# Kernel optimization log

Hardware: AMD Instinct MI355X
Metric: run time of the kernel (lower is better)

Reference implementation:

```python
import jax, jax.numpy as jnp
import numpy as np

VOCAB, EMBED, FILT, LABELS = 30522, 256, 256, 50
B, S = 32, 4096

def setup_inputs() -> dict:
    key = jax.random.key(0)
    k0, k1, k2, k3, k4 = jax.random.split(key, 5)
    return {
        "input_ids": jax.random.randint(k0, (B, S), 0, VOCAB),
        "emb_table": jax.random.normal(k1, (VOCAB, EMBED), dtype=jnp.float32) * 0.02,
        "conv_w": jax.random.normal(k2, (FILT, EMBED, 4), dtype=jnp.float32) * 0.05,  # (out_ch, in_ch, k)
        "conv_b": jnp.zeros((FILT,), dtype=jnp.float32),
        "U_w": jax.random.normal(k3, (LABELS, FILT), dtype=jnp.float32) * 0.05,  # torch Linear weight layout
        "final_w": jax.random.normal(k4, (LABELS, FILT), dtype=jnp.float32) * 0.05,
        "final_b": jnp.zeros((LABELS,), dtype=jnp.float32),
    }

def reference(input_ids, emb_table, conv_w, conv_b, U_w, final_w, final_b):
    # Embedding lookup: (B, S, E) -> NCH layout (B, E, S)
    x = jnp.take(emb_table, input_ids, axis=0).transpose(0, 2, 1)
    # Conv1d(kernel=4, padding=2): output length S+1
    h = jax.lax.conv_general_dilated(
        x, conv_w, window_strides=(1,), padding=[(2, 2)],
        dimension_numbers=("NCH", "OIH", "NCH"))
    H = jnp.tanh(h + conv_b[None, :, None]).transpose(0, 2, 1)  # (B, S+1, F)
    # Per-label attention: softmax over the sequence dimension
    scores = jnp.einsum("bsf,lf->bsl", H, U_w)          # (B, S+1, L)
    alpha = jax.nn.softmax(scores, axis=1)
    m = jnp.einsum("bsl,bsf->blf", alpha, H)             # (B, L, F)
    logits = jnp.sum(m * final_w[None], axis=2) + final_b  # (B, L)
    return logits
```

## Files before the change

### kernel.cpp

```cpp
#include <hip/hip_runtime.h>
#include <hip/hip_bf16.h>
#include <stdint.h>

#define BDIM 32
#define SDIM 4096
#define SP1  4097
#define EDIM 256
#define FDIM 256
#define LDIM 50
#define TTILE 128
#define NT    32

typedef __attribute__((ext_vector_type(8))) short bf16x8v;
typedef __attribute__((ext_vector_type(4))) float f32x4;

__device__ __forceinline__ unsigned short f2bf(float f) {
    union { float f; uint32_t u; } v; v.f = f;
    uint32_t u = v.u;
    uint32_t r = (u + 0x7fffu + ((u >> 16) & 1u)) >> 16;
    return (unsigned short)r;
}

__device__ __forceinline__ float tanh_fast(float x) {
    float e = __expf(2.0f * x);
    float r = __builtin_amdgcn_rcpf(e + 1.0f);
    return fmaf(-2.0f, r, 1.0f);
}

__device__ __forceinline__ uint32_t pack_bf2(float lo, float hi) {
    union { __hip_bfloat162 v; uint32_t u; } cv;
    cv.v = __halves2bfloat162(__float2bfloat16(lo), __float2bfloat16(hi));
    return cv.u;
}

__device__ __forceinline__ void load_lds16(const void* g, uint32_t* l) {
    __builtin_amdgcn_global_load_lds(
        (const __attribute__((address_space(1))) uint32_t*)g,
        (__attribute__((address_space(3))) uint32_t*)l, 16, 0, 0);
}

__global__ void prep_all(const float* __restrict__ emb, const float* __restrict__ conv_w,
                         const float* __restrict__ U_w, const float* __restrict__ final_w,
                         unsigned short* __restrict__ embb, unsigned short* __restrict__ Wb2,
                         unsigned short* __restrict__ W2k, float* __restrict__ Wt01,
                         uint32_t* __restrict__ zp)
{
    int o = blockIdx.x * 256 + threadIdx.x;
    size_t eo = (size_t)o * 8;
    if (eo < (size_t)30522 * 256) {
        float4 v0 = *(const float4*)(emb + eo);
        float4 v1 = *(const float4*)(emb + eo + 4);
        union { unsigned short u[8]; uint4 q; } pk;
        pk.u[0] = f2bf(v0.x); pk.u[1] = f2bf(v0.y); pk.u[2] = f2bf(v0.z); pk.u[3] = f2bf(v0.w);
        pk.u[4] = f2bf(v1.x); pk.u[5] = f2bf(v1.y); pk.u[6] = f2bf(v1.z); pk.u[7] = f2bf(v1.w);
        *(uint4*)(embb + eo) = pk.q;
    }
    if (o < 262144) {
        int kk = o & 1023, f = o >> 10;
        int e = kk & 255, k = kk >> 8;
        int g = kk >> 5, h4 = (kk >> 3) & 3, j = kk & 7;
        Wb2[((size_t)(g * 4 + h4) * 256 + f) * 8 + j] = f2bf(conv_w[f * 1024 + e * 4 + k]);
    }
    if (o < 32768) {
        int j = o & 7, c = (o >> 3) & 127, g = o >> 10;
        int k = g * 8 + j, l = c & 63;
        float v = 0.f;
        if (l < LDIM) v = (c < 64) ? U_w[l * FDIM + k] : final_w[l * FDIM + k];
        W2k[o] = f2bf(v);
    }
    if (o < 65536) {
        int f = o & 255, e = o >> 8;
        Wt01[(size_t)o * 2]     = conv_w[f * 1024 + e * 4];
        Wt01[(size_t)o * 2 + 1] = conv_w[f * 1024 + e * 4 + 1];
    }
    if (o < 128) zp[o] = 0;
}

__global__ __launch_bounds__(256, 2) void fused_kernel(
    const int* __restrict__ ids, const unsigned short* __restrict__ embb,
    const unsigned short* __restrict__ Wb2, const float* __restrict__ conv_b,
    const unsigned short* __restrict__ W2k, const uint32_t* __restrict__ zp,
    float* __restrict__ part)
{
    __shared__ uint32_t xs[132 * 128];

    const int tid  = threadIdx.x;
    const int lane = tid & 63;
    const int wid  = tid >> 6;
    const int b    = blockIdx.y;
    const int tile = blockIdx.x;
    const int t0   = tile * TTILE;
    const int l15  = lane & 15;
    const int hi4  = lane >> 4;
    const int q    = lane & 31;
    const int half = lane >> 5;

    {
        int nid[17];
        #pragma unroll
        for (int j = 0; j < 17; ++j) {
            int r0 = wid * 2 + j * 8;
            int r  = r0 + half;
            int p  = t0 - 2 + r;
            nid[j] = -1;
            if (r0 < 131 && r < 131 && (unsigned)p < SDIM)
                nid[j] = ids[b * SDIM + p];
        }
        const unsigned short* zs = (const unsigned short*)zp + q * 8;
        #pragma unroll
        for (int j = 0; j < 17; ++j) {
            int r0 = wid * 2 + j * 8;
            if (r0 >= 131) continue;
            int r = r0 + half;
            const unsigned short* s = (nid[j] >= 0)
                ? embb + (size_t)nid[j] * EDIM + (((uint32_t)(q * 16) ^ ((uint32_t)(r & 7) << 4)) >> 1)
                : zs;
            load_lds16(s, &xs[r0 * 128]);
        }
    }
    __syncthreads();

    const int fbase = wid * 64;
    const unsigned short* afbase = Wb2 + (size_t)(hi4 * 256 + fbase + l15) * 8;

    f32x4 acc[4][8];
    #pragma unroll
    for (int a = 0; a < 4; ++a)
        #pragma unroll
        for (int n = 0; n < 8; ++n) acc[a][n] = (f32x4){0.f, 0.f, 0.f, 0.f};

    bf16x8v afc[4];
    #pragma unroll
    for (int a = 0; a < 4; ++a) afc[a] = *(const bf16x8v*)(afbase + a * 128);

    #pragma unroll 1
    for (int k = 0; k < 4; ++k) {
        uint32_t bb[8];
        #pragma unroll
        for (int n = 0; n < 8; ++n) {
            int r = n * 16 + l15 + k;
            bb[n] = (uint32_t)(r * 512) ^ (uint32_t)(hi4 * 16) ^ (uint32_t)((r & 7) << 4);
        }
        const unsigned short* afg = afbase + (size_t)k * 65536;
        #pragma unroll
        for (int es = 0; es < 8; ++es) {
            const unsigned short* nxt = (es < 7)
                ? (afg + (size_t)(es + 1) * 8192)
                : (afbase + (size_t)((k + 1) & 3) * 65536);
            bf16x8v afn[4];
            #pragma unroll
            for (int a = 0; a < 4; ++a) afn[a] = *(const bf16x8v*)(nxt + a * 128);

            bf16x8v bfr[8];
            #pragma unroll
            for (int n = 0; n < 8; ++n)
                bfr[n] = *(const bf16x8v*)((const char*)xs + (bb[n] ^ (uint32_t)(es * 64)));

            __builtin_amdgcn_s_setprio(1);
            #pragma unroll
            for (int a = 0; a < 4; ++a)
                #pragma unroll
                for (int n = 0; n < 8; ++n)
                    acc[a][n] = __builtin_amdgcn_mfma_f32_16x16x32_bf16(afc[a], bfr[n], acc[a][n], 0, 0, 0);
            __builtin_amdgcn_s_setprio(0);

            #pragma unroll
            for (int a = 0; a < 4; ++a) afc[a] = afn[a];
        }
    }
    __syncthreads();

    float4 cb[4];
    #pragma unroll
    for (int a = 0; a < 4; ++a)
        cb[a] = *(const float4*)(conv_b + fbase + a * 16 + hi4 * 4);
    #pragma unroll
    for (int n = 0; n < 8; ++n) {
        int tl = n * 16 + l15;
        uint32_t hb = (uint32_t)(tl * 512) ^ (uint32_t)(hi4 * 8)
                    ^ (uint32_t)(fbase * 2) ^ (uint32_t)((tl & 7) << 4);
        #pragma unroll
        for (int a = 0; a < 4; ++a) {
            f32x4 d = acc[a][n];
            uint2 pk;
            pk.x = pack_bf2(tanh_fast(d[0] + cb[a].x), tanh_fast(d[1] + cb[a].y));
            pk.y = pack_bf2(tanh_fast(d[2] + cb[a].z), tanh_fast(d[3] + cb[a].w));
            *(uint2*)((char*)xs + (hb ^ (uint32_t)(a * 32))) = pk;
        }
    }
    __syncthreads();

    const int cbase = wid * 16;
    f32x4 p2[8][2];
    #pragma unroll
    for (int m = 0; m < 8; ++m) { p2[m][0] = (f32x4){0,0,0,0}; p2[m][1] = (f32x4){0,0,0,0}; }

    uint32_t pb[8];
    #pragma unroll
    for (int m = 0; m < 8; ++m) {
        int sl = m * 16 + l15;
        pb[m] = (uint32_t)(sl * 512) ^ (uint32_t)(hi4 * 16) ^ (uint32_t)((sl & 7) << 4);
    }
    const unsigned short* wp0 = W2k + (size_t)(hi4 * 128 + cbase + l15) * 8;

    #pragma unroll
    for (int step = 0; step < 8; ++step) {
        bf16x8v ha[8], w2[2];
        #pragma unroll
        for (int m = 0; m < 8; ++m)
            ha[m] = *(const bf16x8v*)((const char*)xs + (pb[m] ^ (uint32_t)(step * 64)));
        w2[0] = *(const bf16x8v*)(wp0 + step * 4096);
        w2[1] = *(const bf16x8v*)(wp0 + 512 + step * 4096);
        __builtin_amdgcn_s_setprio(1);
        #pragma unroll
        for (int m = 0; m < 8; ++m) {
            p2[m][0] = __builtin_amdgcn_mfma_f32_16x16x32_bf16(ha[m], w2[0], p2[m][0], 0, 0, 0);
            p2[m][1] = __builtin_amdgcn_mfma_f32_16x16x32_bf16(ha[m], w2[1], p2[m][1], 0, 0, 0);
        }
        __builtin_amdgcn_s_setprio(0);
    }

    float mx = -1e30f;
    #pragma unroll
    for (int m = 0; m < 8; ++m)
        #pragma unroll
        for (int i = 0; i < 4; ++i)
            mx = fmaxf(mx, p2[m][0][i]);
    float se = 0.f, st = 0.f;
    #pragma unroll
    for (int m = 0; m < 8; ++m)
        #pragma unroll
        for (int i = 0; i < 4; ++i) {
            float e = __expf(p2[m][0][i] - mx);
            se += e;
            st += e * p2[m][1][i];
        }
    #pragma unroll
    for (int d = 16; d <= 32; d <<= 1) {
        float mo  = __shfl_xor(mx, d);
        float seo = __shfl_xor(se, d);
        float sto = __shfl_xor(st, d);
        float M  = fmaxf(mx, mo);
        float w0 = __expf(mx - M), w1 = __expf(mo - M);
        se = se * w0 + seo * w1;
        st = st * w0 + sto * w1;
        mx = M;
    }
    if (lane < 16) {
        int l = cbase + l15;
        if (l < LDIM) {
            size_t o = (((size_t)b * NT + tile) * LDIM + l) * 3;
            part[o] = mx; part[o + 1] = se; part[o + 2] = st;
        }
    }
}

__global__ __launch_bounds__(256) void final_kernel(
    const int* __restrict__ ids, const float* __restrict__ emb,
    const float* __restrict__ Wt01, const float* __restrict__ conv_b,
    const float* __restrict__ U_w, const float* __restrict__ final_w,
    const float* __restrict__ part, const float* __restrict__ final_b,
    float* __restrict__ out)
{
    __shared__ float x0[EDIM], x1[EDIM], hsh[FDIM], rsc[256], rtv[256];
    const int b = blockIdx.x, t = threadIdx.x;

    {
        int id0 = ids[b * SDIM + 4094];
        int id1 = ids[b * SDIM + 4095];
        x0[t] = emb[(size_t)id0 * EDIM + t];
        x1[t] = emb[(size_t)id1 * EDIM + t];
    }
    __syncthreads();

    {
        const float2* wt = (const float2*)Wt01;
        float a0 = 0.f, a1 = 0.f, a2 = 0.f, a3 = 0.f;
        #pragma unroll 4
        for (int e = 0; e < 256; e += 4) {
            float2 w0 = wt[(e + 0) * 256 + t];
            float2 w1 = wt[(e + 1) * 256 + t];
            float2 w2 = wt[(e + 2) * 256 + t];
            float2 w3 = wt[(e + 3) * 256 + t];
            a0 = fmaf(w0.x, x0[e + 0], fmaf(w0.y, x1[e + 0], a0));
            a1 = fmaf(w1.x, x0[e + 1], fmaf(w1.y, x1[e + 1], a1));
            a2 = fmaf(w2.x, x0[e + 2], fmaf(w2.y, x1[e + 2], a2));
            a3 = fmaf(w3.x, x0[e + 3], fmaf(w3.y, x1[e + 3], a3));
        }
        hsh[t] = tanhf(conv_b[t] + ((a0 + a1) + (a2 + a3)));
    }
    __syncthreads();

    {
        const int l = t & 63, c = t >> 6;
        float sc = 0.f, tv = 0.f;
        if (l < LDIM) {
            const float4* uw = (const float4*)(U_w + (size_t)l * FDIM + c * 64);
            const float4* fw = (const float4*)(final_w + (size_t)l * FDIM + c * 64);
            const float4* hh = (const float4*)(hsh + c * 64);
            #pragma unroll
            for (int i = 0; i < 16; ++i) {
                float4 h = hh[i], u = uw[i], w = fw[i];
                sc = fmaf(h.x, u.x, fmaf(h.y, u.y, fmaf(h.z, u.z, fmaf(h.w, u.w, sc))));
                tv = fmaf(h.x, w.x, fmaf(h.y, w.y, fmaf(h.z, w.z, fmaf(h.w, w.w, tv))));
            }
        }
        rsc[t] = sc; rtv[t] = tv;
    }
    __syncthreads();

    if (t < LDIM) {
        float sc = rsc[t] + rsc[t + 64] + rsc[t + 128] + rsc[t + 192];
        float tv = rtv[t] + rtv[t + 64] + rtv[t + 128] + rtv[t + 192];
        float mx = sc, se = 1.0f, st = tv;
        for (int c = 0; c < NT; ++c) {
            size_t o = (((size_t)b * NT + c) * LDIM + t) * 3;
            float mo = part[o], seo = part[o + 1], sto = part[o + 2];
            float M  = fmaxf(mx, mo);
            float w0 = __expf(mx - M), w1 = __expf(mo - M);
            se = se * w0 + seo * w1;
            st = st * w0 + sto * w1;
            mx = M;
        }
        out[b * LDIM + t] = st / se + final_b[t];
    }
}

extern "C" void kernel_launch(void* const* d_in, const int* in_sizes, int n_in,
                              void* d_out, int out_size, void* d_ws, size_t ws_size,
                              hipStream_t stream)
{
    const int*   ids     = (const int*)d_in[0];
    const float* emb     = (const float*)d_in[1];
    const float* conv_w  = (const float*)d_in[2];
    const float* conv_b  = (const float*)d_in[3];
    const float* U_w     = (const float*)d_in[4];
    const float* final_w = (const float*)d_in[5];
    const float* final_b = (const float*)d_in[6];

    char* ws = (char*)d_ws;
    size_t offE  = 0;
    size_t szE   = (size_t)30522 * 256 * 2;
    size_t offWb = offE + szE;
    size_t szWb  = 256 * 1024 * 2;
    size_t offW2 = offWb + szWb;
    size_t szW2  = 32768 * 2;
    size_t offWt = offW2 + szW2;
    size_t szWt  = 65536 * 2 * 4;
    size_t offZ  = offWt + szWt;
    size_t szZ   = 512;
    size_t offP  = offZ + szZ;

    unsigned short* embb = (unsigned short*)(ws + offE);
    unsigned short* Wb2  = (unsigned short*)(ws + offWb);
    unsigned short* W2k  = (unsigned short*)(ws + offW2);
    float*          Wt01 = (float*)(ws + offWt);
    uint32_t*       zp   = (uint32_t*)(ws + offZ);
    float*          prt  = (float*)(ws + offP);

    prep_all<<<3816, 256, 0, stream>>>(emb, conv_w, U_w, final_w, embb, Wb2, W2k, Wt01, zp);
    fused_kernel<<<dim3(NT, BDIM), 256, 0, stream>>>(ids, embb, Wb2, conv_b, W2k, zp, prt);
    final_kernel<<<BDIM, 256, 0, stream>>>(ids, emb, Wt01, conv_b, U_w, final_w,
                                           prt, final_b, (float*)d_out);
}
```

Baseline: 97.57 us.

## Fold final reduction into fused kernel via last-block atomic counter

Removes the separate final_kernel launch. Each batch gets one extra block that computes the tail-position conv and attention contribution. The last block to arrive, tracked by an atomic counter per batch, merges all partial softmax states and writes the output. This saves one kernel launch and the serialization between kernels, at the cost of threadfences, atomics and an extra block per batch row in the main grid.

After: 166.4 us. +70.6%, slower.

```diff
diff --git a/kernel.cpp b/kernel.cpp
--- a/kernel.cpp
+++ b/kernel.cpp
@@ -39,11 +39,18 @@
         (__attribute__((address_space(3))) uint32_t*)l, 16, 0, 0);
 }
 
+__device__ __forceinline__ void pstore(float* p, float v) {
+    __hip_atomic_store(p, v, __ATOMIC_RELAXED, __HIP_MEMORY_SCOPE_AGENT);
+}
+__device__ __forceinline__ float pload(const float* p) {
+    return __hip_atomic_load(p, __ATOMIC_RELAXED, __HIP_MEMORY_SCOPE_AGENT);
+}
+
 __global__ void prep_all(const float* __restrict__ emb, const float* __restrict__ conv_w,
                          const float* __restrict__ U_w, const float* __restrict__ final_w,
                          unsigned short* __restrict__ embb, unsigned short* __restrict__ Wb2,
                          unsigned short* __restrict__ W2k, float* __restrict__ Wt01,
-                         uint32_t* __restrict__ zp)
+                         uint32_t* __restrict__ zp, int* __restrict__ cnt)
 {
     int o = blockIdx.x * 256 + threadIdx.x;
     size_t eo = (size_t)o * 8;
@@ -74,255 +81,274 @@
         Wt01[(size_t)o * 2 + 1] = conv_w[f * 1024 + e * 4 + 1];
     }
     if (o < 128) zp[o] = 0;
+    if (o < BDIM) cnt[o] = 0;
 }
 
 __global__ __launch_bounds__(256, 2) void fused_kernel(
     const int* __restrict__ ids, const unsigned short* __restrict__ embb,
     const unsigned short* __restrict__ Wb2, const float* __restrict__ conv_b,
     const unsigned short* __restrict__ W2k, const uint32_t* __restrict__ zp,
-    float* __restrict__ part)
+    const float* __restrict__ Wt01, const float* __restrict__ emb,
+    const float* __restrict__ U_w, const float* __restrict__ final_w,
+    const float* __restrict__ final_b, float* __restrict__ part,
+    int* __restrict__ cnt, float* __restrict__ out)
 {
     __shared__ uint32_t xs[132 * 128];
+    __shared__ int lord;
 
     const int tid  = threadIdx.x;
     const int lane = tid & 63;
     const int wid  = tid >> 6;
     const int b    = blockIdx.y;
     const int tile = blockIdx.x;
-    const int t0   = tile * TTILE;
-    const int l15  = lane & 15;
-    const int hi4  = lane >> 4;
-    const int q    = lane & 31;
-    const int half = lane >> 5;
-
-    {
-        int nid[17];
-        #pragma unroll
-        for (int j = 0; j < 17; ++j) {
-            int r0 = wid * 2 + j * 8;
-            int r  = r0 + half;
-            int p  = t0 - 2 + r;
-            nid[j] = -1;
-            if (r0 < 131 && r < 131 && (unsigned)p < SDIM)
-                nid[j] = ids[b * SDIM + p];
-        }
-        const unsigned short* zs = (const unsigned short*)zp + q * 8;
-        #pragma unroll
-        for (int j = 0; j < 17; ++j) {
-            int r0 = wid * 2 + j * 8;
-            if (r0 >= 131) continue;
-            int r = r0 + half;
-            const unsigned short* s = (nid[j] >= 0)
-                ? embb + (size_t)nid[j] * EDIM + (((uint32_t)(q * 16) ^ ((uint32_t)(r & 7) << 4)) >> 1)
-                : zs;
-            load_lds16(s, &xs[r0 * 128]);
-        }
-    }
-    __syncthreads();
-
-    const int fbase = wid * 64;
-    const unsigned short* afbase = Wb2 + (size_t)(hi4 * 256 + fbase + l15) * 8;
-
-    f32x4 acc[4][8];
-    #pragma unroll
-    for (int a = 0; a < 4; ++a)
-        #pragma unroll
-        for (int n = 0; n < 8; ++n) acc[a][n] = (f32x4){0.f, 0.f, 0.f, 0.f};
-
-    bf16x8v afc[4];
-    #pragma unroll
-    for (int a = 0; a < 4; ++a) afc[a] = *(const bf16x8v*)(afbase + a * 128);
-
-    #pragma unroll 1
-    for (int k = 0; k < 4; ++k) {
-        uint32_t bb[8];
+
+    if (tile < NT) {
+        const int t0   = tile * TTILE;
+        const int l15  = lane & 15;
+        const int hi4  = lane >> 4;
+        const int q    = lane & 31;
+        const int half = lane >> 5;
+
+        {
+            int nid[17];
+            #pragma unroll
+            for (int j = 0; j < 17; ++j) {
+                int r0 = wid * 2 + j * 8;
+                int r  = r0 + half;
+                int p  = t0 - 2 + r;
+                nid[j] = -1;
+                if (r0 < 131 && r < 131 && (unsigned)p < SDIM)
+                    nid[j] = ids[b * SDIM + p];
+            }
+            const unsigned short* zs = (const unsigned short*)zp + q * 8;
+            #pragma unroll
+            for (int j = 0; j < 17; ++j) {
+                int r0 = wid * 2 + j * 8;
+                if (r0 >= 131) continue;
+                int r = r0 + half;
+                const unsigned short* s = (nid[j] >= 0)
+                    ? embb + (size_t)nid[j] * EDIM + (((uint32_t)(q * 16) ^ ((uint32_t)(r & 7) << 4)) >> 1)
+                    : zs;
+                load_lds16(s, &xs[r0 * 128]);
+            }
+        }
+        __syncthreads();
+
+        const int fbase = wid * 64;
+        const unsigned short* afbase = Wb2 + (size_t)(hi4 * 256 + fbase + l15) * 8;
+
+        f32x4 acc[4][8];
+        #pragma unroll
+        for (int a = 0; a < 4; ++a)
+            #pragma unroll
+            for (int n = 0; n < 8; ++n) acc[a][n] = (f32x4){0.f, 0.f, 0.f, 0.f};
+
+        bf16x8v afc[4];
+        #pragma unroll
+        for (int a = 0; a < 4; ++a) afc[a] = *(const bf16x8v*)(afbase + a * 128);
+
+        #pragma unroll 1
+        for (int k = 0; k < 4; ++k) {
+            uint32_t bb[8];
+            #pragma unroll
+            for (int n = 0; n < 8; ++n) {
+                int r = n * 16 + l15 + k;
+                bb[n] = (uint32_t)(r * 512) ^ (uint32_t)(hi4 * 16) ^ (uint32_t)((r & 7) << 4);
+            }
+            const unsigned short* afg = afbase + (size_t)k * 65536;
+            #pragma unroll
+            for (int es = 0; es < 8; ++es) {
+                const unsigned short* nxt = (es < 7)
+                    ? (afg + (size_t)(es + 1) * 8192)
+                    : (afbase + (size_t)((k + 1) & 3) * 65536);
+                bf16x8v afn[4];
+                #pragma unroll
+                for (int a = 0; a < 4; ++a) afn[a] = *(const bf16x8v*)(nxt + a * 128);
+
+                bf16x8v bfr[8];
+                #pragma unroll
+                for (int n = 0; n < 8; ++n)
+                    bfr[n] = *(const bf16x8v*)((const char*)xs + (bb[n] ^ (uint32_t)(es * 64)));
+
+                __builtin_amdgcn_s_setprio(1);
+                #pragma unroll
+                for (int a = 0; a < 4; ++a)
+                    #pragma unroll
+                    for (int n = 0; n < 8; ++n)
+                        acc[a][n] = __builtin_amdgcn_mfma_f32_16x16x32_bf16(afc[a], bfr[n], acc[a][n], 0, 0, 0);
+                __builtin_amdgcn_s_setprio(0);
+
+                #pragma unroll
+                for (int a = 0; a < 4; ++a) afc[a] = afn[a];
+            }
+        }
+        __syncthreads();
+
+        float4 cb[4];
+        #pragma unroll
+        for (int a = 0; a < 4; ++a)
+            cb[a] = *(const float4*)(conv_b + fbase + a * 16 + hi4 * 4);
         #pragma unroll
         for (int n = 0; n < 8; ++n) {
-            int r = n * 16 + l15 + k;
-            bb[n] = (uint32_t)(r * 512) ^ (uint32_t)(hi4 * 16) ^ (uint32_t)((r & 7) << 4);
-        }
-        const unsigned short* afg = afbase + (size_t)k * 65536;
-        #pragma unroll
-        for (int es = 0; es < 8; ++es) {
-            const unsigned short* nxt = (es < 7)
-                ? (afg + (size_t)(es + 1) * 8192)
-                : (afbase + (size_t)((k + 1) & 3) * 65536);
-            bf16x8v afn[4];
-            #pragma unroll
-            for (int a = 0; a < 4; ++a) afn[a] = *(const bf16x8v*)(nxt + a * 128);
-
-            bf16x8v bfr[8];
-            #pragma unroll
-            for (int n = 0; n < 8; ++n)
-                bfr[n] = *(const bf16x8v*)((const char*)xs + (bb[n] ^ (uint32_t)(es * 64)));
-
+            int tl = n * 16 + l15;
+            uint32_t hb = (uint32_t)(tl * 512) ^ (uint32_t)(hi4 * 8)
+                        ^ (uint32_t)(fbase * 2) ^ (uint32_t)((tl & 7) << 4);
+            #pragma unroll
+            for (int a = 0; a < 4; ++a) {
+                f32x4 d = acc[a][n];
+                uint2 pk;
+                pk.x = pack_bf2(tanh_fast(d[0] + cb[a].x), tanh_fast(d[1] + cb[a].y));
+                pk.y = pack_bf2(tanh_fast(d[2] + cb[a].z), tanh_fast(d[3] + cb[a].w));
+                *(uint2*)((char*)xs + (hb ^ (uint32_t)(a * 32))) = pk;
+            }
+        }
+        __syncthreads();
+
+        const int cbase = wid * 16;
+        f32x4 p2[8][2];
+        #pragma unroll
+        for (int m = 0; m < 8; ++m) { p2[m][0] = (f32x4){0,0,0,0}; p2[m][1] = (f32x4){0,0,0,0}; }
+
+        uint32_t pb[8];
+        #pragma unroll
+        for (int m = 0; m < 8; ++m) {
+            int sl = m * 16 + l15;
+            pb[m] = (uint32_t)(sl * 512) ^ (uint32_t)(hi4 * 16) ^ (uint32_t)((sl & 7) << 4);
+        }
+        const unsigned short* wp0 = W2k + (size_t)(hi4 * 128 + cbase + l15) * 8;
+
+        #pragma unroll
+        for (int step = 0; step < 8; ++step) {
+            bf16x8v ha[8], w2[2];
+            #pragma unroll
+            for (int m = 0; m < 8; ++m)
+                ha[m] = *(const bf16x8v*)((const char*)xs + (pb[m] ^ (uint32_t)(step * 64)));
+            w2[0] = *(const bf16x8v*)(wp0 + step * 4096);
+            w2[1] = *(const bf16x8v*)(wp0 + 512 + step * 4096);
             __builtin_amdgcn_s_setprio(1);
             #pragma unroll
-            for (int a = 0; a < 4; ++a)
-                #pragma unroll
-                for (int n = 0; n < 8; ++n)
-                    acc[a][n] = __builtin_amdgcn_mfma_f32_16x16x32_bf16(afc[a], bfr[n], acc[a][n], 0, 0, 0);
+            for (int m = 0; m < 8; ++m) {
+                p2[m][0] = __builtin_amdgcn_mfma_f32_16x16x32_bf16(ha[m], w2[0], p2[m][0], 0, 0, 0);
+                p2[m][1] = __builtin_amdgcn_mfma_f32_16x16x32_bf16(ha[m], w2[1], p2[m][1], 0, 0, 0);
+            }
             __builtin_amdgcn_s_setprio(0);
-
-            #pragma unroll
-            for (int a = 0; a < 4; ++a) afc[a] = afn[a];
-        }
-    }
-    __syncthreads();
-
-    float4 cb[4];
-    #pragma unroll
-    for (int a = 0; a < 4; ++a)
-        cb[a] = *(const float4*)(conv_b + fbase + a * 16 + hi4 * 4);
-    #pragma unroll
-    for (int n = 0; n < 8; ++n) {
-        int tl = n * 16 + l15;
-        uint32_t hb = (uint32_t)(tl * 512) ^ (uint32_t)(hi4 * 8)
-                    ^ (uint32_t)(fbase * 2) ^ (uint32_t)((tl & 7) << 4);
-        #pragma unroll
-        for (int a = 0; a < 4; ++a) {
-            f32x4 d = acc[a][n];
-            uint2 pk;
-            pk.x = pack_bf2(tanh_fast(d[0] + cb[a].x), tanh_fast(d[1] + cb[a].y));
-            pk.y = pack_bf2(tanh_fast(d[2] + cb[a].z), tanh_fast(d[3] + cb[a].w));
-            *(uint2*)((char*)xs + (hb ^ (uint32_t)(a * 32))) = pk;
-        }
-    }
-    __syncthreads();
-
-    const int cbase = wid * 16;
-    f32x4 p2[8][2];
-    #pragma unroll
-    for (int m = 0; m < 8; ++m) { p2[m][0] = (f32x4){0,0,0,0}; p2[m][1] = (f32x4){0,0,0,0}; }
-
-    uint32_t pb[8];
-    #pragma unroll
-    for (int m = 0; m < 8; ++m) {
-        int sl = m * 16 + l15;
-        pb[m] = (uint32_t)(sl * 512) ^ (uint32_t)(hi4 * 16) ^ (uint32_t)((sl & 7) << 4);
-    }
-    const unsigned short* wp0 = W2k + (size_t)(hi4 * 128 + cbase + l15) * 8;
-
-    #pragma unroll
-    for (int step = 0; step < 8; ++step) {
-        bf16x8v ha[8], w2[2];
+        }
+
+        float mx = -1e30f;
         #pragma unroll
         for (int m = 0; m < 8; ++m)
-            ha[m] = *(const bf16x8v*)((const char*)xs + (pb[m] ^ (uint32_t)(step * 64)));
-        w2[0] = *(const bf16x8v*)(wp0 + step * 4096);
-        w2[1] = *(const bf16x8v*)(wp0 + 512 + step * 4096);
-        __builtin_amdgcn_s_setprio(1);
-        #pragma unroll
-        for (int m = 0; m < 8; ++m) {
-            p2[m][0] = __builtin_amdgcn_mfma_f32_16x16x32_bf16(ha[m], w2[0], p2[m][0], 0, 0, 0);
-            p2[m][1] = __builtin_amdgcn_mfma_f32_16x16x32_bf16(ha[m], w2[1], p2[m][1], 0, 0, 0);
-        }
-        __builtin_amdgcn_s_setprio(0);
-    }
-
-    float mx = -1e30f;
-    #pragma unroll
-    for (int m = 0; m < 8; ++m)
-        #pragma unroll
-        for (int i = 0; i < 4; ++i)
-            mx = fmaxf(mx, p2[m][0][i]);
-    float se = 0.f, st = 0.f;
-    #pragma unroll
-    for (int m = 0; m < 8; ++m)
-        #pragma unroll
-        for (int i = 0; i < 4; ++i) {
-            float e = __expf(p2[m][0][i] - mx);
-            se += e;
-            st += e * p2[m][1][i];
-        }
-    #pragma unroll
-    for (int d = 16; d <= 32; d <<= 1) {
-        float mo  = __shfl_xor(mx, d);
-        float seo = __shfl_xor(se, d);
-        float sto = __shfl_xor(st, d);
-        float M  = fmaxf(mx, mo);
-        float w0 = __expf(mx - M), w1 = __expf(mo - M);
-        se = se * w0 + seo * w1;
-        st = st * w0 + sto * w1;
-        mx = M;
-    }
-    if (lane < 16) {
-        int l = cbase + l15;
-        if (l < LDIM) {
-            size_t o = (((size_t)b * NT + tile) * LDIM + l) * 3;
-            part[o] = mx; part[o + 1] = se; part[o + 2] = st;
-        }
-    }
-}
-
-__global__ __launch_bounds__(256) void final_kernel(
-    const int* __restrict__ ids, const float* __restrict__ emb,
-    const float* __restrict__ Wt01, const float* __restrict__ conv_b,
-    const float* __restrict__ U_w, const float* __restrict__ final_w,
-    const float* __restrict__ part, const float* __restrict__ final_b,
-    float* __restrict__ out)
-{
-    __shared__ float x0[EDIM], x1[EDIM], hsh[FDIM], rsc[256], rtv[256];
-    const int b = blockIdx.x, t = threadIdx.x;
-
-    {
-        int id0 = ids[b * SDIM + 4094];
-        int id1 = ids[b * SDIM + 4095];
-        x0[t] = emb[(size_t)id0 * EDIM + t];
-        x1[t] = emb[(size_t)id1 * EDIM + t];
-    }
-    __syncthreads();
-
-    {
-        const float2* wt = (const float2*)Wt01;
-        float a0 = 0.f, a1 = 0.f, a2 = 0.f, a3 = 0.f;
-        #pragma unroll 4
-        for (int e = 0; e < 256; e += 4) {
-            float2 w0 = wt[(e + 0) * 256 + t];
-            float2 w1 = wt[(e + 1) * 256 + t];
-            float2 w2 = wt[(e + 2) * 256 + t];
-            float2 w3 = wt[(e + 3) * 256 + t];
-            a0 = fmaf(w0.x, x0[e + 0], fmaf(w0.y, x1[e + 0], a0));
-            a1 = fmaf(w1.x, x0[e + 1], fmaf(w1.y, x1[e + 1], a1));
-            a2 = fmaf(w2.x, x0[e + 2], fmaf(w2.y, x1[e + 2], a2));
-            a3 = fmaf(w3.x, x0[e + 3], fmaf(w3.y, x1[e + 3], a3));
-        }
-        hsh[t] = tanhf(conv_b[t] + ((a0 + a1) + (a2 + a3)));
-    }
-    __syncthreads();
-
-    {
-        const int l = t & 63, c = t >> 6;
-        float sc = 0.f, tv = 0.f;
-        if (l < LDIM) {
-            const float4* uw = (const float4*)(U_w + (size_t)l * FDIM + c * 64);
-            const float4* fw = (const float4*)(final_w + (size_t)l * FDIM + c * 64);
-            const float4* hh = (const float4*)(hsh + c * 64);
-            #pragma unroll
-            for (int i = 0; i < 16; ++i) {
-                float4 h = hh[i], u = uw[i], w = fw[i];
-                sc = fmaf(h.x, u.x, fmaf(h.y, u.y, fmaf(h.z, u.z, fmaf(h.w, u.w, sc))));
-                tv = fmaf(h.x, w.x, fmaf(h.y, w.y, fmaf(h.z, w.z, fmaf(h.w, w.w, tv))));
-            }
-        }
-        rsc[t] = sc; rtv[t] = tv;
-    }
-    __syncthreads();
-
-    if (t < LDIM) {
-        float sc = rsc[t] + rsc[t + 64] + rsc[t + 128] + rsc[t + 192];
-        float tv = rtv[t] + rtv[t + 64] + rtv[t + 128] + rtv[t + 192];
-        float mx = sc, se = 1.0f, st = tv;
-        for (int c = 0; c < NT; ++c) {
-            size_t o = (((size_t)b * NT + c) * LDIM + t) * 3;
-            float mo = part[o], seo = part[o + 1], sto = part[o + 2];
+            #pragma unroll
+            for (int i = 0; i < 4; ++i)
+                mx = fmaxf(mx, p2[m][0][i]);
+        float se = 0.f, st = 0.f;
+        #pragma unroll
+        for (int m = 0; m < 8; ++m)
+            #pragma unroll
+            for (int i = 0; i < 4; ++i) {
+                float e = __expf(p2[m][0][i] - mx);
+                se += e;
+                st += e * p2[m][1][i];
+            }
+        #pragma unroll
+        for (int d = 16; d <= 32; d <<= 1) {
+            float mo  = __shfl_xor(mx, d);
+            float seo = __shfl_xor(se, d);
+            float sto = __shfl_xor(st, d);
             float M  = fmaxf(mx, mo);
             float w0 = __expf(mx - M), w1 = __expf(mo - M);
             se = se * w0 + seo * w1;
             st = st * w0 + sto * w1;
             mx = M;
         }
-        out[b * LDIM + t] = st / se + final_b[t];
+        if (lane < 16) {
+            int l = cbase + l15;
+            if (l < LDIM) {
+                size_t o = (((size_t)b * (NT + 1) + tile) * LDIM + l) * 3;
+                pstore(&part[o], mx); pstore(&part[o + 1], se); pstore(&part[o + 2], st);
+            }
+        }
+    } else {
+        float* fs  = (float*)xs;
+        float* x0  = fs;
+        float* x1  = fs + 256;
+        float* hsh = fs + 512;
+        float* rsc = fs + 768;
+        float* rtv = fs + 1024;
+        const int t = tid;
+
+        {
+            int id0 = ids[b * SDIM + 4094];
+            int id1 = ids[b * SDIM + 4095];
+            x0[t] = emb[(size_t)id0 * EDIM + t];
+            x1[t] = emb[(size_t)id1 * EDIM + t];
+        }
+        __syncthreads();
+
+        {
+            const float2* wt = (const float2*)Wt01;
+            float a0 = 0.f, a1 = 0.f, a2 = 0.f, a3 = 0.f;
+            #pragma unroll 4
+            for (int e = 0; e < 256; e += 4) {
+                float2 w0 = wt[(e + 0) * 256 + t];
+                float2 w1 = wt[(e + 1) * 256 + t];
+                float2 w2 = wt[(e + 2) * 256 + t];
+                float2 w3 = wt[(e + 3) * 256 + t];
+                a0 = fmaf(w0.x, x0[e + 0], fmaf(w0.y, x1[e + 0], a0));
+                a1 = fmaf(w1.x, x0[e + 1], fmaf(w1.y, x1[e + 1], a1));
+                a2 = fmaf(w2.x, x0[e + 2], fmaf(w2.y, x1[e + 2], a2));
+                a3 = fmaf(w3.x, x0[e + 3], fmaf(w3.y, x1[e + 3], a3));
+            }
+            hsh[t] = tanhf(conv_b[t] + ((a0 + a1) + (a2 + a3)));
+        }
+        __syncthreads();
+
+        {
+            const int l = t & 63, c = t >> 6;
+            float sc = 0.f, tv = 0.f;
+            if (l < LDIM) {
+                const float4* uw = (const float4*)(U_w + (size_t)l * FDIM + c * 64);
+                const float4* fw = (const float4*)(final_w + (size_t)l * FDIM + c * 64);
+                const float4* hh = (const float4*)(hsh + c * 64);
+                #pragma unroll
+                for (int i = 0; i < 16; ++i) {
+                    float4 h = hh[i], u = uw[i], w = fw[i];
+                    sc = fmaf(h.x, u.x, fmaf(h.y, u.y, fmaf(h.z, u.z, fmaf(h.w, u.w, sc))));
+                    tv = fmaf(h.x, w.x, fmaf(h.y, w.y, fmaf(h.z, w.z, fmaf(h.w, w.w, tv))));
+                }
+            }
+            rsc[t] = sc; rtv[t] = tv;
+        }
+        __syncthreads();
+
+        if (t < LDIM) {
+            float sc = rsc[t] + rsc[t + 64] + rsc[t + 128] + rsc[t + 192];
+            float tv = rtv[t] + rtv[t + 64] + rtv[t + 128] + rtv[t + 192];
+            size_t o = (((size_t)b * (NT + 1) + NT) * LDIM + t) * 3;
+            pstore(&part[o], sc); pstore(&part[o + 1], 1.0f); pstore(&part[o + 2], tv);
+        }
+    }
+
+    __threadfence();
+    __syncthreads();
+    if (tid == 0) lord = atomicAdd(&cnt[b], 1);
+    __syncthreads();
+    if (lord == NT) {
+        __threadfence();
+        if (tid < LDIM) {
+            float mx = -1e30f, se = 0.f, st = 0.f;
+            for (int c = 0; c <= NT; ++c) {
+                size_t o = (((size_t)b * (NT + 1) + c) * LDIM + tid) * 3;
+                float mo  = pload(&part[o]);
+                float seo = pload(&part[o + 1]);
+                float sto = pload(&part[o + 2]);
+                float M  = fmaxf(mx, mo);
+                float w0 = __expf(mx - M), w1 = __expf(mo - M);
+                se = se * w0 + seo * w1;
+                st = st * w0 + sto * w1;
+                mx = M;
+            }
+            out[b * LDIM + tid] = st / se + final_b[tid];
+        }
     }
 }
 
@@ -350,6 +376,8 @@
     size_t offZ  = offWt + szWt;
     size_t szZ   = 512;
     size_t offP  = offZ + szZ;
+    size_t szP   = (size_t)BDIM * (NT + 1) * LDIM * 3 * 4;
+    size_t offC  = offP + szP;
 
     unsigned short* embb = (unsigned short*)(ws + offE);
     unsigned short* Wb2  = (unsigned short*)(ws + offWb);
@@ -357,9 +385,10 @@
     float*          Wt01 = (float*)(ws + offWt);
     uint32_t*       zp   = (uint32_t*)(ws + offZ);
     float*          prt  = (float*)(ws + offP);
-
-    prep_all<<<3816, 256, 0, stream>>>(emb, conv_w, U_w, final_w, embb, Wb2, W2k, Wt01, zp);
-    fused_kernel<<<dim3(NT, BDIM), 256, 0, stream>>>(ids, embb, Wb2, conv_b, W2k, zp, prt);
-    final_kernel<<<BDIM, 256, 0, stream>>>(ids, emb, Wt01, conv_b, U_w, final_w,
-                                           prt, final_b, (float*)d_out);
-}
+    int*            cnt  = (int*)(ws + offC);
+
+    prep_all<<<3816, 256, 0, stream>>>(emb, conv_w, U_w, final_w, embb, Wb2, W2k, Wt01, zp, cnt);
+    fused_kernel<<<dim3(NT + 1, BDIM), 256, 0, stream>>>(
+        ids, embb, Wb2, conv_b, W2k, zp, Wt01, emb, U_w, final_w, final_b,
+        prt, cnt, (float*)d_out);
+}
```
